# Kernel optimization log

Hardware: AMD Instinct MI355X
Metric: run time of the kernel (lower is better)

Reference implementation:

```python
import jax, jax.numpy as jnp
import numpy as np

B, T, N, H, E, LH, OUT, D = 64, 12, 325, 64, 32, 128, 12, 1
META_OFF = 65  # x[..., :1] is the signal, x[..., 65:] is the 32-dim temporal meta input


def _mlp(meta, W1, b1, W2, b2):
    # meta: (B,E); W1: (4,E,LH); W2: (4,LH,O) -> (4,B,O); 4 = gates g,i,f,o
    h = jax.nn.relu(jnp.einsum('be,geh->gbh', meta, W1) + b1[:, None, :])
    return jnp.einsum('gbh,gho->gbo', h, W2) + b2[:, None, :]


def setup_inputs() -> dict:
    key = jax.random.key(0)
    ks = jax.random.split(key, 16)
    s = lambda k, shape: jax.random.normal(k, shape, dtype=jnp.float32) * 0.05
    return {
        'x': jax.random.normal(ks[0], (B, T, N, 1 + 64 + E), dtype=jnp.float32),
        'lwx_W1': s(ks[1], (4, E, LH)), 'lwx_b1': s(ks[2], (4, LH)),
        'lwx_W2': s(ks[3], (4, LH, D * H)), 'lwx_b2': s(ks[4], (4, D * H)),
        'lwh_W1': s(ks[5], (4, E, LH)), 'lwh_b1': s(ks[6], (4, LH)),
        'lwh_W2': s(ks[7], (4, LH, H * H)), 'lwh_b2': s(ks[8], (4, H * H)),
        'lb_W1': s(ks[9], (4, E, LH)), 'lb_b1': s(ks[10], (4, LH)),
        'lb_W2': s(ks[11], (4, LH, H)), 'lb_b2': s(ks[12], (4, H)),
        'fc1_W': s(ks[13], (H, H // 2)), 'fc1_b': jnp.zeros((H // 2,), jnp.float32),
        'fc2_W': s(ks[14], (H // 2, OUT * D)), 'fc2_b': jnp.zeros((OUT * D,), jnp.float32),
    }


def reference(x, lwx_W1, lwx_b1, lwx_W2, lwx_b2,
              lwh_W1, lwh_b1, lwh_W2, lwh_b2,
              lb_W1, lb_b1, lb_W2, lb_b2,
              fc1_W, fc1_b, fc2_W, fc2_b):
    batch = x.shape[0]
    meta = jnp.mean(x[:, :, 0, META_OFF:], axis=1)  # (B,E)
    xs = jnp.transpose(x[..., :D], (1, 0, 2, 3))    # (T,B,N,D)

    Wx = _mlp(meta, lwx_W1, lwx_b1, lwx_W2, lwx_b2).reshape(4, batch, D, H)
    Wh = _mlp(meta, lwh_W1, lwh_b1, lwh_W2, lwh_b2).reshape(4, batch, H, H)
    b = _mlp(meta, lb_W1, lb_b1, lb_W2, lb_b2).reshape(4, batch, 1, H)

    def step(carry, xt):
        h, c = carry
        # (4,B,N,H): per-batch weights -> batched matmuls for all 4 gates
        z = (jnp.einsum('bnd,gbdh->gbnh', xt, Wx)
             + jnp.einsum('bnh,gbhk->gbnk', h, Wh) + b)
        g = jnp.tanh(z[0])
        i = jax.nn.sigmoid(z[1])
        f = jax.nn.sigmoid(z[2])
        o = jax.nn.sigmoid(z[3])
        c = g * i + c * f
        h = jnp.tanh(c) * o
        return (h, c), None

    # h0=c0=0 reproduces the torch t==0 special case exactly
    h0 = jnp.zeros((batch, N, H), x.dtype)
    (h, _), _ = jax.lax.scan(step, (h0, h0), xs)

    out = jax.nn.relu(h)
    out = jax.nn.relu(out @ fc1_W + fc1_b) @ fc2_W + fc2_b  # (B,N,OUT*D)
    out = out.reshape(batch, N, OUT, D)
    return jnp.transpose(out, (0, 2, 1, 3))  # (B,OUT,N,D)
```

## Files before the change

### kernel.cpp

```cpp
#include <hip/hip_runtime.h>
#include <stdint.h>

#define TT 12
#define NN 325
#define HH 64
#define EE 32
#define LHH 128
#define OO 12
#define CIN 97
#define MOFF 65
#define BB 64

typedef __attribute__((ext_vector_type(8))) short bf8;
typedef __attribute__((ext_vector_type(4))) float f4;

__device__ __forceinline__ float sigf(float x) {
  return __builtin_amdgcn_rcpf(1.f + __builtin_amdgcn_exp2f(-1.4426950408889634f * x));
}
__device__ __forceinline__ float tanhfast(float x) {
  return 1.f - 2.f * __builtin_amdgcn_rcpf(1.f + __builtin_amdgcn_exp2f(2.8853900817779268f * x));
}
__device__ __forceinline__ unsigned short f2bf(float f) {
  unsigned int u = __float_as_uint(f);
  u += 0x7fffu + ((u >> 16) & 1u);
  return (unsigned short)(u >> 16);
}
__device__ __forceinline__ float bf2f(unsigned short s) {
  return __uint_as_float(((unsigned int)s) << 16);
}

__global__ __launch_bounds__(256) void k_meta(
    const float* __restrict__ x,
    const float* __restrict__ xw1, const float* __restrict__ xb1,
    const float* __restrict__ xw2, const float* __restrict__ xb2,
    const float* __restrict__ hw1, const float* __restrict__ hb1,
    const float* __restrict__ bw1, const float* __restrict__ bb1,
    const float* __restrict__ bw2, const float* __restrict__ bb2,
    float* __restrict__ hid_ws, float* __restrict__ wx_ws,
    float* __restrict__ bg_ws)
{
  const int b = blockIdx.x, tid = threadIdx.x;
  __shared__ float mpart[TT][EE];
  __shared__ float meta_s[EE];
  __shared__ float hidx_s[512], hidb_s[512];

  for (int idx = tid; idx < TT * EE; idx += 256) {
    const int t = idx >> 5, e = idx & 31;
    mpart[t][e] = x[(size_t)((b * TT + t) * NN) * CIN + MOFF + e];
  }
  __syncthreads();
  if (tid < EE) {
    float s = 0.f;
    #pragma unroll
    for (int t = 0; t < TT; ++t) s += mpart[t][tid];
    meta_s[tid] = s * (1.f / 12.f);
  }
  __syncthreads();

  for (int idx = tid; idx < 1536; idx += 256) {
    const int mlp = idx >> 9, rem = idx & 511;
    const int g = rem >> 7, l = rem & 127;
    const float* W1 = (mlp == 0) ? xw1 : ((mlp == 1) ? hw1 : bw1);
    const float* B1 = (mlp == 0) ? xb1 : ((mlp == 1) ? hb1 : bb1);
    float a = B1[rem];
    const float* w = W1 + g * (EE * LHH) + l;
    #pragma unroll
    for (int e = 0; e < EE; ++e) a = fmaf(meta_s[e], w[e * LHH], a);
    a = fmaxf(a, 0.f);
    if (mlp == 0) hidx_s[rem] = a;
    else if (mlp == 2) hidb_s[rem] = a;
    else hid_ws[g * (BB * LHH) + b * LHH + l] = a;
  }
  __syncthreads();

  {
    const int g = tid >> 6;
    const int h = tid & 63;
    float ax = xb2[tid];
    float ab = bb2[tid];
    const float* wxp = xw2 + (size_t)g * (LHH * HH) + h;
    const float* wbp = bw2 + (size_t)g * (LHH * HH) + h;
    const float* hx = hidx_s + g * LHH;
    const float* hb = hidb_s + g * LHH;
    #pragma unroll 8
    for (int l = 0; l < LHH; ++l) {
      ax = fmaf(hx[l], wxp[l * HH], ax);
      ab = fmaf(hb[l], wbp[l * HH], ab);
    }
    wx_ws[b * 256 + tid] = ax;
    bg_ws[b * 256 + tid] = ab;
  }
}

__global__ __launch_bounds__(256) void k_wh(
    const float* __restrict__ x,
    const float* __restrict__ hw2, const float* __restrict__ hb2,
    const float* __restrict__ hid_ws, unsigned short* __restrict__ whb,
    float* __restrict__ xg)
{
  const int g = blockIdx.x >> 6, i = blockIdx.x & 63, tid = threadIdx.x;
  __shared__ float hs[BB][132];
  __shared__ float w2s[LHH][HH];

  {
    const int base = blockIdx.x * 976;
    #pragma unroll
    for (int kk = 0; kk < 4; ++kk) {
      const int flat = base + kk * 256 + tid;
      if (flat < BB * TT * NN) {
        const int b = flat / (TT * NN);
        const int r = flat - b * (TT * NN);
        const int t = r / NN;
        const int n = r - t * NN;
        xg[flat] = x[(size_t)((b * TT + t) * NN + n) * CIN];
      }
    }
  }

  for (int idx = tid; idx < BB * LHH; idx += 256)
    hs[idx >> 7][idx & 127] = hid_ws[g * (BB * LHH) + idx];
  for (int idx = tid; idx < LHH * HH; idx += 256)
    w2s[idx >> 6][idx & 63] = hw2[(size_t)(g * LHH + (idx >> 6)) * 4096 + i * 64 + (idx & 63)];
  __syncthreads();

  const int rg = tid >> 4, cg = tid & 15;
  const int b0 = rg * 4, j0 = cg * 4;
  float acc[4][4] = {};
  for (int l = 0; l < LHH; l += 4) {
    f4 hv[4];
    #pragma unroll
    for (int rr = 0; rr < 4; ++rr) hv[rr] = *(const f4*)&hs[b0 + rr][l];
    #pragma unroll
    for (int ll = 0; ll < 4; ++ll) {
      const f4 wv = *(const f4*)&w2s[l + ll][j0];
      #pragma unroll
      for (int rr = 0; rr < 4; ++rr)
        #pragma unroll
        for (int jj = 0; jj < 4; ++jj)
          acc[rr][jj] = fmaf(hv[rr][ll], wv[jj], acc[rr][jj]);
    }
  }

  const int kh = i >> 5, quad = (i >> 3) & 3, j8 = i & 7;
  #pragma unroll
  for (int rr = 0; rr < 4; ++rr) {
    const int b = b0 + rr;
    #pragma unroll
    for (int jj = 0; jj < 4; ++jj) {
      const int j = j0 + jj;
      const float v = acc[rr][jj] + hb2[g * 4096 + i * 64 + j];
      const int col = g * 64 + j;
      const int nt = col >> 4, c16 = col & 15;
      const int lane = quad * 16 + c16;
      whb[(size_t)((b * 32 + kh * 16 + nt) * 64 + lane) * 8 + j8] = f2bf(v);
    }
  }
}

__global__ __launch_bounds__(256, 3) void k_lstm(
    const float* __restrict__ xg, const float* __restrict__ wx_ws,
    const float* __restrict__ bg_ws, const unsigned short* __restrict__ whb,
    const float* __restrict__ fc1W, const float* __restrict__ fc1b,
    const float* __restrict__ fc2W, const float* __restrict__ fc2b,
    float* __restrict__ out)
{
  const int rb = blockIdx.x, b = blockIdx.y, tid = threadIdx.x;
  const int wave = tid >> 6, lane = tid & 63, quad = lane >> 4, c16 = lane & 15;
  const int n0 = rb * 32;

  __shared__ __align__(16) unsigned short Hs[2][2][16][72];
  __shared__ float Xs[TT][32];
  __shared__ float fc1s[HH * 32];
  __shared__ float fc2s[32 * OO];
  __shared__ float HIDs[32][36];
  __shared__ float fc1bs[32];
  __shared__ float fc2bs[OO];

  for (int idx = tid; idx < TT * 32; idx += 256) {
    const int t = idx >> 5, r = idx & 31, n = n0 + r;
    Xs[t][r] = (n < NN) ? xg[b * (TT * NN) + t * NN + n] : 0.f;
  }
  for (int idx = tid; idx < HH * 32; idx += 256) fc1s[idx] = fc1W[idx];
  for (int idx = tid; idx < 32 * OO; idx += 256) fc2s[idx] = fc2W[idx];
  if (tid < 32) fc1bs[tid] = fc1b[tid];
  if (tid < OO) fc2bs[tid] = fc2b[tid];

  float wxv[4], bgv[4];
  #pragma unroll
  for (int g = 0; g < 4; ++g) {
    wxv[g] = wx_ws[b * 256 + g * 64 + wave * 16 + c16];
    bgv[g] = bg_ws[b * 256 + g * 64 + wave * 16 + c16];
  }
  bf8 wf[2][4];
  #pragma unroll
  for (int kh = 0; kh < 2; ++kh)
    #pragma unroll
    for (int g = 0; g < 4; ++g)
      wf[kh][g] = *(const bf8*)(whb + (size_t)((b * 32 + kh * 16 + g * 4 + wave) * 64 + lane) * 8);

  float cst[2][4];
  #pragma unroll
  for (int ta = 0; ta < 2; ++ta)
    #pragma unroll
    for (int r = 0; r < 4; ++r) cst[ta][r] = 0.f;

  __syncthreads();

  #pragma unroll 1
  for (int t = 0; t < TT; ++t) {
    bf8 af[2][2];
    if (t > 0) {
      #pragma unroll
      for (int ta = 0; ta < 2; ++ta) {
        af[ta][0] = *(const bf8*)&Hs[(t - 1) & 1][ta][c16][quad * 8];
        af[ta][1] = *(const bf8*)&Hs[(t - 1) & 1][ta][c16][32 + quad * 8];
      }
    }
    f4 ac[2][4];
    #pragma unroll
    for (int ta = 0; ta < 2; ++ta) {
      float xr[4];
      #pragma unroll
      for (int r = 0; r < 4; ++r) xr[r] = Xs[t][ta * 16 + quad * 4 + r];
      #pragma unroll
      for (int g = 0; g < 4; ++g)
        #pragma unroll
        for (int r = 0; r < 4; ++r)
          ac[ta][g][r] = fmaf(xr[r], wxv[g], bgv[g]);
    }
    if (t > 0) {
      #pragma unroll
      for (int ta = 0; ta < 2; ++ta)
        #pragma unroll
        for (int g = 0; g < 4; ++g) {
          ac[ta][g] = __builtin_amdgcn_mfma_f32_16x16x32_bf16(af[ta][0], wf[0][g], ac[ta][g], 0, 0, 0);
          ac[ta][g] = __builtin_amdgcn_mfma_f32_16x16x32_bf16(af[ta][1], wf[1][g], ac[ta][g], 0, 0, 0);
        }
    }
    #pragma unroll
    for (int ta = 0; ta < 2; ++ta)
      #pragma unroll
      for (int r = 0; r < 4; ++r) {
        const float gg = tanhfast(ac[ta][0][r]);
        const float ii = sigf(ac[ta][1][r]);
        const float ff = sigf(ac[ta][2][r]);
        const float oo = sigf(ac[ta][3][r]);
        const float cc = fmaf(gg, ii, cst[ta][r] * ff);
        cst[ta][r] = cc;
        const float hh = tanhfast(cc) * oo;
        Hs[t & 1][ta][quad * 4 + r][wave * 16 + c16] = f2bf(hh);
      }
    __syncthreads();
  }

  {
    const int row32 = tid & 31, uu = tid >> 5;
    const int ta = row32 >> 4, row = row32 & 15;
    float hacc[4];
    #pragma unroll
    for (int j = 0; j < 4; ++j) hacc[j] = fc1bs[uu * 4 + j];
    #pragma unroll
    for (int kc = 0; kc < 8; ++kc) {
      const bf8 hv = *(const bf8*)&Hs[1][ta][row][kc * 8];
      #pragma unroll
      for (int j8 = 0; j8 < 8; ++j8) {
        const float hk = fmaxf(bf2f((unsigned short)hv[j8]), 0.f);
        const int k = kc * 8 + j8;
        #pragma unroll
        for (int j = 0; j < 4; ++j)
          hacc[j] = fmaf(hk, fc1s[k * 32 + uu * 4 + j], hacc[j]);
      }
    }
    #pragma unroll
    for (int j = 0; j < 4; ++j)
      HIDs[row32][uu * 4 + j] = fmaxf(hacc[j], 0.f);
  }
  __syncthreads();
  for (int idx = tid; idx < 32 * OO; idx += 256) {
    const int o = idx >> 5, row32 = idx & 31;
    float a = fc2bs[o];
    #pragma unroll
    for (int k = 0; k < 32; ++k)
      a = fmaf(HIDs[row32][k], fc2s[k * OO + o], a);
    const int n = n0 + row32;
    if (n < NN)
      out[b * (OO * NN) + o * NN + n] = a;
  }
}

extern "C" void kernel_launch(void* const* d_in, const int* in_sizes, int n_in,
                              void* d_out, int out_size, void* d_ws, size_t ws_size,
                              hipStream_t stream) {
  const float* x    = (const float*)d_in[0];
  const float* xw1  = (const float*)d_in[1];
  const float* xb1  = (const float*)d_in[2];
  const float* xw2  = (const float*)d_in[3];
  const float* xb2  = (const float*)d_in[4];
  const float* hw1  = (const float*)d_in[5];
  const float* hb1  = (const float*)d_in[6];
  const float* hw2  = (const float*)d_in[7];
  const float* hb2  = (const float*)d_in[8];
  const float* bw1  = (const float*)d_in[9];
  const float* bb1  = (const float*)d_in[10];
  const float* bw2  = (const float*)d_in[11];
  const float* bb2  = (const float*)d_in[12];
  const float* fc1W = (const float*)d_in[13];
  const float* fc1b = (const float*)d_in[14];
  const float* fc2W = (const float*)d_in[15];
  const float* fc2b = (const float*)d_in[16];
  float* out = (float*)d_out;

  float* ws = (float*)d_ws;
  float* hid_ws = ws;
  float* wx_ws  = ws + 32768;
  float* bg_ws  = ws + 49152;
  float* xg_ws  = ws + 65536;
  unsigned short* whb = (unsigned short*)(ws + 65536 + BB * TT * NN);

  k_meta<<<64, 256, 0, stream>>>(x, xw1, xb1, xw2, xb2, hw1, hb1, bw1, bb1,
                                 bw2, bb2, hid_ws, wx_ws, bg_ws);
  k_wh<<<256, 256, 0, stream>>>(x, hw2, hb2, hid_ws, whb, xg_ws);
  k_lstm<<<dim3(11, 64), 256, 0, stream>>>(xg_ws, wx_ws, bg_ws, whb,
                                           fc1W, fc1b, fc2W, fc2b, out);
}
```

Measured before the change: 224.5 us.

## Split meta and Wh-generation kernels across more blocks per gate and batch quarter

k_meta now launches one block per (gate, batch) instead of per batch. Its second-layer dot product is split into four partial sums that are reduced in shared memory. k_wh launches four times more blocks, each handling a quarter of the batch with a 2x2 register tile instead of 4x4. The aim is to fill more CUs in these small prologue kernels, at the cost of recomputing meta and reloading the hw2 tile in every block.

```diff
diff --git a/kernel.cpp b/kernel.cpp
--- a/kernel.cpp
+++ b/kernel.cpp
@@ -39,10 +39,11 @@
     float* __restrict__ hid_ws, float* __restrict__ wx_ws,
     float* __restrict__ bg_ws)
 {
-  const int b = blockIdx.x, tid = threadIdx.x;
+  const int g = blockIdx.x >> 6, b = blockIdx.x & 63, tid = threadIdx.x;
   __shared__ float mpart[TT][EE];
   __shared__ float meta_s[EE];
-  __shared__ float hidx_s[512], hidb_s[512];
+  __shared__ float hid3[3][LHH];
+  __shared__ float psum[2][4][HH];
 
   for (int idx = tid; idx < TT * EE; idx += 256) {
     const int t = idx >> 5, e = idx & 31;
@@ -57,38 +58,41 @@
   }
   __syncthreads();
 
-  for (int idx = tid; idx < 1536; idx += 256) {
-    const int mlp = idx >> 9, rem = idx & 511;
-    const int g = rem >> 7, l = rem & 127;
+  for (int idx = tid; idx < 3 * LHH; idx += 256) {
+    const int mlp = idx >> 7, l = idx & 127;
     const float* W1 = (mlp == 0) ? xw1 : ((mlp == 1) ? hw1 : bw1);
     const float* B1 = (mlp == 0) ? xb1 : ((mlp == 1) ? hb1 : bb1);
-    float a = B1[rem];
-    const float* w = W1 + g * (EE * LHH) + l;
+    float a = B1[g * LHH + l];
+    const float* w = W1 + (size_t)g * (EE * LHH) + l;
     #pragma unroll
     for (int e = 0; e < EE; ++e) a = fmaf(meta_s[e], w[e * LHH], a);
     a = fmaxf(a, 0.f);
-    if (mlp == 0) hidx_s[rem] = a;
-    else if (mlp == 2) hidb_s[rem] = a;
-    else hid_ws[g * (BB * LHH) + b * LHH + l] = a;
+    hid3[mlp][l] = a;
+    if (mlp == 1) hid_ws[g * (BB * LHH) + b * LHH + l] = a;
   }
   __syncthreads();
 
   {
-    const int g = tid >> 6;
-    const int h = tid & 63;
-    float ax = xb2[tid];
-    float ab = bb2[tid];
+    const int part = tid >> 6, h = tid & 63;
+    float ax = 0.f, ab = 0.f;
     const float* wxp = xw2 + (size_t)g * (LHH * HH) + h;
     const float* wbp = bw2 + (size_t)g * (LHH * HH) + h;
-    const float* hx = hidx_s + g * LHH;
-    const float* hb = hidb_s + g * LHH;
-    #pragma unroll 8
-    for (int l = 0; l < LHH; ++l) {
-      ax = fmaf(hx[l], wxp[l * HH], ax);
-      ab = fmaf(hb[l], wbp[l * HH], ab);
-    }
-    wx_ws[b * 256 + tid] = ax;
-    bg_ws[b * 256 + tid] = ab;
+    #pragma unroll
+    for (int ll = 0; ll < 32; ++ll) {
+      const int l = part * 32 + ll;
+      ax = fmaf(hid3[0][l], wxp[l * HH], ax);
+      ab = fmaf(hid3[2][l], wbp[l * HH], ab);
+    }
+    psum[0][part][h] = ax;
+    psum[1][part][h] = ab;
+  }
+  __syncthreads();
+  if (tid < 128) {
+    const int isb = tid >> 6, h = tid & 63;
+    const float bias = (isb ? bb2 : xb2)[g * HH + h];
+    const float a = bias + psum[isb][0][h] + psum[isb][1][h]
+                         + psum[isb][2][h] + psum[isb][3][h];
+    (isb ? bg_ws : wx_ws)[b * 256 + g * 64 + h] = a;
   }
 }
 
@@ -98,55 +102,52 @@
     const float* __restrict__ hid_ws, unsigned short* __restrict__ whb,
     float* __restrict__ xg)
 {
-  const int g = blockIdx.x >> 6, i = blockIdx.x & 63, tid = threadIdx.x;
-  __shared__ float hs[BB][132];
+  const int g = blockIdx.x >> 8, i = (blockIdx.x >> 2) & 63, bq = blockIdx.x & 3;
+  const int tid = threadIdx.x;
+  __shared__ float hs[16][132];
   __shared__ float w2s[LHH][HH];
 
   {
-    const int base = blockIdx.x * 976;
-    #pragma unroll
-    for (int kk = 0; kk < 4; ++kk) {
-      const int flat = base + kk * 256 + tid;
-      if (flat < BB * TT * NN) {
-        const int b = flat / (TT * NN);
-        const int r = flat - b * (TT * NN);
-        const int t = r / NN;
-        const int n = r - t * NN;
-        xg[flat] = x[(size_t)((b * TT + t) * NN + n) * CIN];
-      }
-    }
-  }
-
-  for (int idx = tid; idx < BB * LHH; idx += 256)
-    hs[idx >> 7][idx & 127] = hid_ws[g * (BB * LHH) + idx];
+    const int flat = blockIdx.x * 244 + tid;
+    if (tid < 244 && flat < BB * TT * NN) {
+      const int b = flat / (TT * NN);
+      const int r = flat - b * (TT * NN);
+      const int t = r / NN;
+      const int n = r - t * NN;
+      xg[flat] = x[(size_t)((b * TT + t) * NN + n) * CIN];
+    }
+  }
+
+  for (int idx = tid; idx < 16 * LHH; idx += 256)
+    hs[idx >> 7][idx & 127] =
+        hid_ws[g * (BB * LHH) + (bq * 16 + (idx >> 7)) * LHH + (idx & 127)];
   for (int idx = tid; idx < LHH * HH; idx += 256)
-    w2s[idx >> 6][idx & 63] = hw2[(size_t)(g * LHH + (idx >> 6)) * 4096 + i * 64 + (idx & 63)];
-  __syncthreads();
-
-  const int rg = tid >> 4, cg = tid & 15;
-  const int b0 = rg * 4, j0 = cg * 4;
-  float acc[4][4] = {};
+    w2s[idx >> 6][idx & 63] =
+        hw2[(size_t)(g * LHH + (idx >> 6)) * 4096 + i * 64 + (idx & 63)];
+  __syncthreads();
+
+  const int r0 = (tid >> 5) * 2, j0 = (tid & 31) * 2;
+  float acc[2][2] = {};
   for (int l = 0; l < LHH; l += 4) {
-    f4 hv[4];
-    #pragma unroll
-    for (int rr = 0; rr < 4; ++rr) hv[rr] = *(const f4*)&hs[b0 + rr][l];
+    const f4 h0 = *(const f4*)&hs[r0][l];
+    const f4 h1 = *(const f4*)&hs[r0 + 1][l];
     #pragma unroll
     for (int ll = 0; ll < 4; ++ll) {
-      const f4 wv = *(const f4*)&w2s[l + ll][j0];
-      #pragma unroll
-      for (int rr = 0; rr < 4; ++rr)
-        #pragma unroll
-        for (int jj = 0; jj < 4; ++jj)
-          acc[rr][jj] = fmaf(hv[rr][ll], wv[jj], acc[rr][jj]);
+      const float w0 = w2s[l + ll][j0];
+      const float w1 = w2s[l + ll][j0 + 1];
+      acc[0][0] = fmaf(h0[ll], w0, acc[0][0]);
+      acc[0][1] = fmaf(h0[ll], w1, acc[0][1]);
+      acc[1][0] = fmaf(h1[ll], w0, acc[1][0]);
+      acc[1][1] = fmaf(h1[ll], w1, acc[1][1]);
     }
   }
 
   const int kh = i >> 5, quad = (i >> 3) & 3, j8 = i & 7;
   #pragma unroll
-  for (int rr = 0; rr < 4; ++rr) {
-    const int b = b0 + rr;
-    #pragma unroll
-    for (int jj = 0; jj < 4; ++jj) {
+  for (int rr = 0; rr < 2; ++rr) {
+    const int b = bq * 16 + r0 + rr;
+    #pragma unroll
+    for (int jj = 0; jj < 2; ++jj) {
       const int j = j0 + jj;
       const float v = acc[rr][jj] + hb2[g * 4096 + i * 64 + j];
       const int col = g * 64 + j;
@@ -317,9 +318,9 @@
   float* xg_ws  = ws + 65536;
   unsigned short* whb = (unsigned short*)(ws + 65536 + BB * TT * NN);
 
-  k_meta<<<64, 256, 0, stream>>>(x, xw1, xb1, xw2, xb2, hw1, hb1, bw1, bb1,
-                                 bw2, bb2, hid_ws, wx_ws, bg_ws);
-  k_wh<<<256, 256, 0, stream>>>(x, hw2, hb2, hid_ws, whb, xg_ws);
+  k_meta<<<256, 256, 0, stream>>>(x, xw1, xb1, xw2, xb2, hw1, hb1, bw1, bb1,
+                                  bw2, bb2, hid_ws, wx_ws, bg_ws);
+  k_wh<<<1024, 256, 0, stream>>>(x, hw2, hb2, hid_ws, whb, xg_ws);
   k_lstm<<<dim3(11, 64), 256, 0, stream>>>(xg_ws, wx_ws, bg_ws, whb,
                                            fc1W, fc1b, fc2W, fc2b, out);
 }
```

Result: faster. 214.5 us (-4.4%).
